# Kernel tuning notes

Hardware: AMD Instinct MI355X
Metric: run time of the kernel (lower is better)

## Reference

```python
import jax, jax.numpy as jnp
import numpy as np

EPS = 1e-5

def _conv3x3(x, w):
    # x: [n,c,h,w], w: [o,c,3,3], stride 1, padding 1 (SAME)
    return jax.lax.conv_general_dilated(x, w, (1, 1), 'SAME',
                                        dimension_numbers=('NCHW', 'OIHW', 'NCHW'))

def _bn(x, g, b, m, v):
    # inference-mode BatchNorm2d with running stats
    s = g / jnp.sqrt(v + EPS)
    return x * s[:, None, None] + (b - m * s)[:, None, None]

def _lrelu(x):
    return jnp.where(x > 0, x, 0.2 * x)

def _conv1x1(x, w, b):
    # w: [o,c] (1x1 conv kernel collapsed)
    return jnp.einsum('nchw,oc->nohw', x, w) + b[:, None, None]

def _conv_relu(x, w, g, b, m, v):
    return _lrelu(_bn(_conv3x3(x, w), g, b, m, v))

def _pam(f, Wq, bq, Wk, bk, Wv, bv, alpha):
    n, c, h, w = f.shape
    hw = h * w
    q = _conv1x1(f, Wq, bq).reshape(n, -1, hw)   # [n,cr,hw]
    k = _conv1x1(f, Wk, bk).reshape(n, -1, hw)   # [n,cr,hw]
    # attention[i,j] over spatial tokens, softmax along j
    attn = jax.nn.softmax(jnp.einsum('nci,ncj->nij', q, k), axis=-1)  # [n,hw,hw]
    v = _conv1x1(f, Wv, bv).reshape(n, c, hw)    # [n,c,hw]
    # torch: bmm(v, attn^T) -> out[:, :, i] = sum_j v[:, :, j] * attn[i, j]
    out = jnp.einsum('ncj,nij->nci', v, attn).reshape(n, c, h, w)
    return alpha * out + f

def _cam(f, W1, b1, W2, b2):
    s = jnp.mean(f, axis=(2, 3), keepdims=True)  # AdaptiveAvgPool2d(1)
    s = _lrelu(_conv1x1(s, W1, b1))
    s = jax.nn.sigmoid(_conv1x1(s, W2, b2))
    return f * s

def _upx2(x):
    n, c, h, w = x.shape
    return jax.image.resize(x, (n, c, 2 * h, 2 * w), 'bilinear')

def setup_inputs() -> dict:
    key = jax.random.key(0)
    ks = jax.random.split(key, 16)
    N, C, H, W_ = 4, 512, 64, 64
    CR, NC = C // 8, 64
    f32 = jnp.float32
    def nrm(k, shape, s=0.05):
        return jax.random.normal(k, shape, f32) * s
    return {
        'x': jax.random.normal(ks[0], (N, C, H, W_), f32),
        'W_pam_in': nrm(ks[1], (C, C, 3, 3)),
        'pam_gamma': jnp.ones((C,), f32), 'pam_beta': jnp.zeros((C,), f32),
        'pam_mean': nrm(ks[2], (C,)), 'pam_var': jax.random.uniform(ks[3], (C,), f32) + 0.5,
        'Wq': nrm(ks[4], (CR, C)), 'bq': jnp.zeros((CR,), f32),
        'Wk': nrm(ks[5], (CR, C)), 'bk': jnp.zeros((CR,), f32),
        'Wv': nrm(ks[6], (C, C)), 'bv': jnp.zeros((C,), f32),
        'alpha': nrm(ks[7], (1,), 1.0),
        'W_pam_out': nrm(ks[8], (NC, C)), 'b_pam_out': jnp.zeros((NC,), f32),
        'W_cam_in': nrm(ks[9], (C, C, 3, 3)),
        'cam_gamma': jnp.ones((C,), f32), 'cam_beta': jnp.zeros((C,), f32),
        'cam_mean': nrm(ks[10], (C,)), 'cam_var': jax.random.uniform(ks[11], (C,), f32) + 0.5,
        'Wc1': nrm(ks[12], (CR, C)), 'bc1': jnp.zeros((CR,), f32),
        'Wc2': nrm(ks[13], (C, CR)), 'bc2': jnp.zeros((C,), f32),
        'W_cam_out': nrm(ks[14], (NC, C)), 'b_cam_out': jnp.zeros((NC,), f32),
    }

def reference(x, W_pam_in, pam_gamma, pam_beta, pam_mean, pam_var,
              Wq, bq, Wk, bk, Wv, bv, alpha, W_pam_out, b_pam_out,
              W_cam_in, cam_gamma, cam_beta, cam_mean, cam_var,
              Wc1, bc1, Wc2, bc2, W_cam_out, b_cam_out):
    pam_feat = _conv_relu(x, W_pam_in, pam_gamma, pam_beta, pam_mean, pam_var)
    pam_feat = _pam(pam_feat, Wq, bq, Wk, bk, Wv, bv, alpha)
    pam_feat = _upx2(_conv1x1(pam_feat, W_pam_out, b_pam_out))
    cam_feat = _conv_relu(x, W_cam_in, cam_gamma, cam_beta, cam_mean, cam_var)
    cam_feat = _cam(cam_feat, Wc1, bc1, Wc2, bc2)
    cam_feat = _upx2(_conv1x1(cam_feat, W_cam_out, b_cam_out))
    return pam_feat + cam_feat
```

## Files before the change

kernel.cpp:

```cpp
#include <hip/hip_runtime.h>
#include <hip/hip_bf16.h>
#include <math.h>

#define N_  4
#define C_  512
#define H_  64
#define W_  64
#define HW_ 4096
#define CR_ 64
#define NC_ 64
#define EPSV 1e-5f

typedef __attribute__((ext_vector_type(8))) __bf16 bf16x8;
typedef __attribute__((ext_vector_type(4))) float f32x4;
typedef __hip_bfloat16 bf16s;

__device__ __forceinline__ unsigned short bfb(float f) {
    union { bf16s h; unsigned short u; } cv;
    cv.h = __float2bfloat16(f);
    return cv.u;
}

__device__ __forceinline__ float b2f(unsigned short h) {
    union { unsigned u; float f; } c; c.u = ((unsigned)h) << 16; return c.f;
}

__device__ __forceinline__ float ex2(float x) {
    return __builtin_amdgcn_exp2f(x);
}

__device__ __forceinline__ int swz8(int row, int ch) {
    return row * 64 + ((ch ^ (row & 7)) << 3);
}

__global__ __launch_bounds__(256) void k_prep(
    const float* __restrict__ x,
    const float* __restrict__ Wpam, const float* __restrict__ Wcam,
    const float* __restrict__ Wq, const float* __restrict__ Wk,
    const float* __restrict__ Wv, const float* __restrict__ Wpo,
    const float* __restrict__ Wco,
    bf16s* __restrict__ xbT,
    bf16s* __restrict__ wbp, bf16s* __restrict__ wbp2,
    bf16s* __restrict__ Wqb, bf16s* __restrict__ Wkb,
    bf16s* __restrict__ Wvb, bf16s* __restrict__ Wpob,
    bf16s* __restrict__ Wcob, float* __restrict__ s0)
{
    __shared__ float xs[64][65];
    const int b = blockIdx.x;
    if (b >= 19976) {
        const int idx = b - 19976;
        const int n   = idx >> 9;
        const int rem = idx & 511;
        const int p0  = (rem & 63) * 64;
        const int c0  = (rem >> 6) * 64;
        const int tid = threadIdx.x;
        for (int e = tid; e < 4096; e += 256) {
            int ci = e >> 6, pi = e & 63;
            xs[ci][pi] = x[((size_t)(n*C_ + c0 + ci))*HW_ + p0 + pi];
        }
        __syncthreads();
        for (int e = tid; e < 4096; e += 256) {
            int pi = e >> 6, ci = e & 63;
            xbT[((size_t)n*HW_ + p0 + pi)*C_ + c0 + ci] =
                __float2bfloat16(xs[ci][pi]);
        }
        return;
    }
    long e = (long)b * 256 + threadIdx.x;
    if (e < 2359296) {
        int c = e & 511; int r = e >> 9;
        int tap = r % 9; int o = r / 9;
        wbp[e] = __float2bfloat16(Wpam[((size_t)o*C_ + c)*9 + tap]);
        return;
    }
    e -= 2359296;
    if (e < 2359296) {
        int c = e & 511; int r = e >> 9;
        int tap = r % 9; int o = r / 9;
        wbp2[e] = __float2bfloat16(Wcam[((size_t)o*C_ + c)*9 + tap]);
        return;
    }
    e -= 2359296;
    if (e < 32768) { Wqb[e] = __float2bfloat16(Wq[e]); return; }
    e -= 32768;
    if (e < 32768) { Wkb[e] = __float2bfloat16(Wk[e]); return; }
    e -= 32768;
    if (e < 262144) { Wvb[e] = __float2bfloat16(Wv[e]); return; }
    e -= 262144;
    if (e < 32768) { Wpob[e] = __float2bfloat16(Wpo[e]); return; }
    e -= 32768;
    if (e < 32768) { Wcob[e] = __float2bfloat16(Wco[e]); return; }
    e -= 32768;
    if (e < 2048) s0[e] = 0.f;
}

__global__ __launch_bounds__(256, 3) void k_conv3x3_mfma(
    const bf16s* __restrict__ xbT,
    const bf16s* __restrict__ wb,  const bf16s* __restrict__ wb2,
    const float* __restrict__ gamma,  const float* __restrict__ beta,
    const float* __restrict__ mean,   const float* __restrict__ var,
    const float* __restrict__ gamma2, const float* __restrict__ beta2,
    const float* __restrict__ mean2,  const float* __restrict__ var2,
    bf16s* __restrict__ featT, bf16s* __restrict__ featT2,
    float* __restrict__ csum)
{
    __shared__ bf16s aL[3][128][36];
    __shared__ bf16s bL[132][36];
    const int tid = threadIdx.x;
    const int lid = blockIdx.x + (blockIdx.y << 5) + (blockIdx.z << 8);
    const int xcd = lid & 7;
    const int half = xcd >> 2;
    const int n    = xcd & 3;
    const int w8   = lid >> 3;
    const int o0 = (w8 >> 5) * 128;
    const int pt = w8 & 31;
    const int y0 = pt * 2;
    const bf16s* wbs = half ? wb2 : wb;
    const float* gm = half ? gamma2 : gamma;
    const float* bt = half ? beta2  : beta;
    const float* mn = half ? mean2  : mean;
    const float* vr = half ? var2   : var;
    bf16s* ft = half ? featT2 : featT;
    const int lane = tid & 63;
    const int wid  = tid >> 6;
    const int wr = wid >> 1, wc = wid & 1;
    const int lr = lane & 15, cb = lane >> 4;

    const int ao  = tid >> 2;
    const int ac  = (tid & 3) * 8;
    const int t0  = tid >> 2;
    const int t1  = t0 + 64;
    const int t2  = t0 + 128;
    const int ry1 = t1 >= 66 ? 1 : 0;
    const int xi1 = t1 - (ry1 ? 66 : 0);

    f32x4 acc[4][4];
#pragma unroll
    for (int i = 0; i < 4; ++i)
#pragma unroll
        for (int j = 0; j < 4; ++j) acc[i][j] = (f32x4){0.f,0.f,0.f,0.f};

    int4 pA0, pA1, pA2, pA3, pA4, pA5, pB0, pB1, pB2;

#define CONV_AADDR(DXI, OHALF, C0, DYI) \
    (const int4*)(wbs + ((size_t)(o0 + (OHALF) + ao)*9 + (DYI)*3 + (DXI))*C_ + (C0) + ac)

#define CONV_BLOAD(DST, RY, XI, C0, DYI, VALID)                               \
    {                                                                         \
        int row_ = y0 + (DYI) - 1 + (RY);                                     \
        int xc_  = (XI) - 1;                                                  \
        int4 v_ = {0,0,0,0};                                                  \
        if ((VALID) && row_ >= 0 && row_ < H_ && xc_ >= 0 && xc_ < W_)        \
            v_ = *(const int4*)(xbT +                                         \
                ((size_t)n*HW_ + row_*W_ + xc_)*C_ + (C0) + ac);              \
        DST = v_;                                                             \
    }

#define CONV_ISSUE(C0, DYI)                                                   \
    {                                                                         \
        pA0 = *CONV_AADDR(0,  0, C0, DYI);                                    \
        pA1 = *CONV_AADDR(0, 64, C0, DYI);                                    \
        pA2 = *CONV_AADDR(1,  0, C0, DYI);                                    \
        pA3 = *CONV_AADDR(1, 64, C0, DYI);                                    \
        pA4 = *CONV_AADDR(2,  0, C0, DYI);                                    \
        pA5 = *CONV_AADDR(2, 64, C0, DYI);                                    \
        CONV_BLOAD(pB0, 0, t0, C0, DYI, 1)                                    \
        CONV_BLOAD(pB1, ry1, xi1, C0, DYI, 1)                                 \
        CONV_BLOAD(pB2, 1, t2 - 66, C0, DYI, tid < 16)                        \
    }

    CONV_ISSUE(0, 0)
    int c0 = 0, dyi = 0;
    for (int it = 0; it < 48; ++it) {
        *(int4*)&aL[0][ao][ac]      = pA0;
        *(int4*)&aL[0][64 + ao][ac] = pA1;
        *(int4*)&aL[1][ao][ac]      = pA2;
        *(int4*)&aL[1][64 + ao][ac] = pA3;
        *(int4*)&aL[2][ao][ac]      = pA4;
        *(int4*)&aL[2][64 + ao][ac] = pA5;
        *(int4*)&bL[t0][ac] = pB0;
        *(int4*)&bL[t1][ac] = pB1;
        if (tid < 16) *(int4*)&bL[t2][ac] = pB2;
        __syncthreads();
        int nd = dyi + 1, nc = c0;
        if (nd == 3) { nd = 0; nc += 32; }
        if (it < 47) CONV_ISSUE(nc, nd)
#pragma unroll
        for (int dxi = 0; dxi < 3; ++dxi) {
            bf16x8 af[4], bfv[4];
#pragma unroll
            for (int fm = 0; fm < 4; ++fm)
                af[fm] = *(const bf16x8*)&aL[dxi][wr*64 + fm*16 + lr][cb*8];
#pragma unroll
            for (int fn = 0; fn < 4; ++fn) {
                int pg = wc*64 + fn*16 + lr;
                int ry = pg >> 6, xc = pg & 63;
                bfv[fn] = *(const bf16x8*)&bL[ry*66 + xc + dxi][cb*8];
            }
#pragma unroll
            for (int fm = 0; fm < 4; ++fm)
#pragma unroll
                for (int fn = 0; fn < 4; ++fn)
                    acc[fm][fn] = __builtin_amdgcn_mfma_f32_16x16x32_bf16(
                        af[fm], bfv[fn], acc[fm][fn], 0, 0, 0);
        }
        __syncthreads();
        c0 = nc; dyi = nd;
    }
#undef CONV_ISSUE
#undef CONV_BLOAD
#undef CONV_AADDR
#pragma unroll
    for (int fm = 0; fm < 4; ++fm) {
        float sc[4], sh[4];
        const int obase = o0 + wr*64 + fm*16 + cb*4;
#pragma unroll
        for (int r = 0; r < 4; ++r) {
            int o = obase + r;
            sc[r] = gm[o] * rsqrtf(vr[o] + EPSV);
            sh[r] = bt[o] - mn[o]*sc[r];
        }
        float ps[4] = {0.f, 0.f, 0.f, 0.f};
#pragma unroll
        for (int fn = 0; fn < 4; ++fn) {
            int pg = wc*64 + fn*16 + lr;
            int p  = pt*128 + pg;
            float vv[4];
#pragma unroll
            for (int r = 0; r < 4; ++r) {
                float t = fmaf(acc[fm][fn][r], sc[r], sh[r]);
                vv[r] = t > 0.f ? t : 0.2f*t;
                ps[r] += vv[r];
            }
            uint2 u;
            u.x = (unsigned)bfb(vv[0]) | ((unsigned)bfb(vv[1]) << 16);
            u.y = (unsigned)bfb(vv[2]) | ((unsigned)bfb(vv[3]) << 16);
            *(uint2*)&ft[((size_t)n*HW_ + p)*C_ + obase] = u;
        }
        if (half) {
#pragma unroll
            for (int r = 0; r < 4; ++r) {
                float s = ps[r];
                s += __shfl_xor(s, 1);
                s += __shfl_xor(s, 2);
                s += __shfl_xor(s, 4);
                s += __shfl_xor(s, 8);
                if (lr == 0) atomicAdd(&csum[n*C_ + obase + r], s);
            }
        }
    }
}

__global__ __launch_bounds__(256, 2) void k_gemm_qkv(
    const bf16s* __restrict__ Wqk, const bf16s* __restrict__ Wv,
    const bf16s* __restrict__ Bt,
    const float* __restrict__ bq, const float* __restrict__ bk,
    const float* __restrict__ bv,
    bf16s* __restrict__ qkb, bf16s* __restrict__ vb)
{
    __shared__ bf16s aL[64][36];
    __shared__ bf16s bL[256][36];
    const int tid = threadIdx.x;
    const int flat = blockIdx.x + (blockIdx.y << 4) + blockIdx.z * 160;
    const int k8 = flat & 7;
    const int n  = k8 >> 1;
    const int xh = k8 & 1;
    const int w8 = flat >> 3;
    const int yy = w8 % 10;
    const int p0 = ((((w8 / 10) << 1) | xh)) << 8;
    const bool isqk = (yy < 2);
    const int o0 = isqk ? yy*64 : (yy - 2)*64;
    const bf16s* A = isqk ? Wqk : Wv;
    const int lane = tid & 63;
    const int wid  = tid >> 6;
    const int lr = lane & 15, cb = lane >> 4;
    const int arow = tid >> 2, ach = (tid & 3) * 8;

    f32x4 acc[4][4];
#pragma unroll
    for (int i = 0; i < 4; ++i)
#pragma unroll
        for (int j = 0; j < 4; ++j) acc[i][j] = (f32x4){0.f,0.f,0.f,0.f};

    int4 pA, pB0, pB1, pB2, pB3;

#define GEMM_ISSUE(C0)                                                        \
    {                                                                         \
        pA = *(const int4*)&A[(size_t)(o0 + arow)*C_ + (C0) + ach];           \
        pB0 = *(const int4*)&Bt[((size_t)n*HW_ + p0 + arow      )*C_ + (C0) + ach]; \
        pB1 = *(const int4*)&Bt[((size_t)n*HW_ + p0 + arow +  64)*C_ + (C0) + ach]; \
        pB2 = *(const int4*)&Bt[((size_t)n*HW_ + p0 + arow + 128)*C_ + (C0) + ach]; \
        pB3 = *(const int4*)&Bt[((size_t)n*HW_ + p0 + arow + 192)*C_ + (C0) + ach]; \
    }

    GEMM_ISSUE(0)
    for (int c0 = 0; c0 < C_; c0 += 32) {
        *(int4*)&aL[arow][ach] = pA;
        *(int4*)&bL[arow      ][ach] = pB0;
        *(int4*)&bL[arow +  64][ach] = pB1;
        *(int4*)&bL[arow + 128][ach] = pB2;
        *(int4*)&bL[arow + 192][ach] = pB3;
        __syncthreads();
        if (c0 + 32 < C_) GEMM_ISSUE(c0 + 32)
        bf16x8 af[4], bfv[4];
#pragma unroll
        for (int fo = 0; fo < 4; ++fo)
            af[fo] = *(const bf16x8*)&aL[fo*16 + lr][cb*8];
#pragma unroll
        for (int fp = 0; fp < 4; ++fp)
            bfv[fp] = *(const bf16x8*)&bL[wid*64 + fp*16 + lr][cb*8];
#pragma unroll
        for (int fo = 0; fo < 4; ++fo)
#pragma unroll
            for (int fp = 0; fp < 4; ++fp)
                acc[fo][fp] = __builtin_amdgcn_mfma_f32_16x16x32_bf16(
                    af[fo], bfv[fp], acc[fo][fp], 0, 0, 0);
        __syncthreads();
    }
#undef GEMM_ISSUE
#pragma unroll
    for (int fo = 0; fo < 4; ++fo) {
        const int obase = o0 + fo*16 + cb*4;
        const bool isq = isqk && !(obase >> 6);
        const float* bp = isqk ? ((obase >> 6) ? bk : bq) : bv;
        const int bofs = isqk ? (obase & 63) : obase;
        float bv4[4];
#pragma unroll
        for (int r = 0; r < 4; ++r) bv4[r] = bp[bofs + r];
#pragma unroll
        for (int fp = 0; fp < 4; ++fp) {
            int p = p0 + wid*64 + fp*16 + lr;
            float v[4];
#pragma unroll
            for (int r = 0; r < 4; ++r) {
                v[r] = acc[fo][fp][r] + bv4[r];
                if (isq) v[r] *= 1.44269504f;
            }
            if (isqk) {
                uint2 u;
                u.x = (unsigned)bfb(v[0]) | ((unsigned)bfb(v[1]) << 16);
                u.y = (unsigned)bfb(v[2]) | ((unsigned)bfb(v[3]) << 16);
                size_t base = (((size_t)((obase >> 6) * N_ + n))*HW_ + p)*64
                              + (obase & 63);
                *(uint2*)&qkb[base] = u;
            } else {
#pragma unroll
                for (int r = 0; r < 4; ++r)
                    vb[((size_t)(n*C_ + obase + r))*HW_ + p] =
                        __float2bfloat16(v[r]);
            }
        }
    }
}

__global__ __launch_bounds__(256, 2) void k_gemm_tail(
    const bf16s* __restrict__ Wpob, const bf16s* __restrict__ Wcob,
    const bf16s* __restrict__ featT, const bf16s* __restrict__ featT2,
    const float* __restrict__ b_pam, const float* __restrict__ b_cam,
    const float* __restrict__ s0, const float* __restrict__ Wc1,
    const float* __restrict__ bc1, const float* __restrict__ Wc2,
    const float* __restrict__ bc2,
    float* __restrict__ pam_low, float* __restrict__ cam_low)
{
    __shared__ bf16s aL[64][36];
    __shared__ bf16s bL[256][36];
    __shared__ float s2s[C_];
    __shared__ float s1s[CR_];
    const int tid = threadIdx.x;
    const int half = blockIdx.y;
    const int n  = blockIdx.z;
    const int p0 = blockIdx.x * 256;
    const bf16s* A = half ? Wcob : Wpob;
    const bf16s* Bt = half ? featT2 : featT;
    const float* bias = half ? b_cam : b_pam;
    float* outp = half ? cam_low : pam_low;
    const int lane = tid & 63;
    const int wid  = tid >> 6;
    const int lr = lane & 15, cb = lane >> 4;
    const int arow = tid >> 2, ach = (tid & 3) * 8;

    if (half) {
        if (tid < CR_) {
            float a = 0.f;
            for (int c = 0; c < C_; ++c)
                a = fmaf(Wc1[(size_t)tid*C_ + c], s0[n*C_ + c] * (1.f/HW_), a);
            a += bc1[tid];
            s1s[tid] = a > 0.f ? a : 0.2f*a;
        }
        __syncthreads();
        for (int c = tid; c < C_; c += 256) {
            float bb = 0.f;
            for (int i = 0; i < CR_; ++i)
                bb = fmaf(Wc2[(size_t)c*CR_ + i], s1s[i], bb);
            bb += bc2[c];
            s2s[c] = 1.f / (1.f + __expf(-bb));
        }
        __syncthreads();
    }

    f32x4 acc[4][4];
#pragma unroll
    for (int i = 0; i < 4; ++i)
#pragma unroll
        for (int j = 0; j < 4; ++j) acc[i][j] = (f32x4){0.f,0.f,0.f,0.f};

    int4 pA, pB0, pB1, pB2, pB3;

#define GEMM_ISSUE(C0)                                                        \
    {                                                                         \
        pA = *(const int4*)&A[(size_t)arow*C_ + (C0) + ach];                  \
        pB0 = *(const int4*)&Bt[((size_t)n*HW_ + p0 + arow      )*C_ + (C0) + ach]; \
        pB1 = *(const int4*)&Bt[((size_t)n*HW_ + p0 + arow +  64)*C_ + (C0) + ach]; \
        pB2 = *(const int4*)&Bt[((size_t)n*HW_ + p0 + arow + 128)*C_ + (C0) + ach]; \
        pB3 = *(const int4*)&Bt[((size_t)n*HW_ + p0 + arow + 192)*C_ + (C0) + ach]; \
    }

    GEMM_ISSUE(0)
    for (int c0 = 0; c0 < C_; c0 += 32) {
        if (half) {
            const bf16s* sp = (const bf16s*)&pA;
            bf16s tmp[8];
#pragma unroll
            for (int u = 0; u < 8; ++u)
                tmp[u] = __float2bfloat16(
                    __bfloat162float(sp[u]) * s2s[c0 + ach + u]);
            *(int4*)&aL[arow][ach] = *(int4*)tmp;
        } else {
            *(int4*)&aL[arow][ach] = pA;
        }
        *(int4*)&bL[arow      ][ach] = pB0;
        *(int4*)&bL[arow +  64][ach] = pB1;
        *(int4*)&bL[arow + 128][ach] = pB2;
        *(int4*)&bL[arow + 192][ach] = pB3;
        __syncthreads();
        if (c0 + 32 < C_) GEMM_ISSUE(c0 + 32)
        bf16x8 af[4], bfv[4];
#pragma unroll
        for (int fo = 0; fo < 4; ++fo)
            af[fo] = *(const bf16x8*)&aL[fo*16 + lr][cb*8];
#pragma unroll
        for (int fp = 0; fp < 4; ++fp)
            bfv[fp] = *(const bf16x8*)&bL[wid*64 + fp*16 + lr][cb*8];
#pragma unroll
        for (int fo = 0; fo < 4; ++fo)
#pragma unroll
            for (int fp = 0; fp < 4; ++fp)
                acc[fo][fp] = __builtin_amdgcn_mfma_f32_16x16x32_bf16(
                    af[fo], bfv[fp], acc[fo][fp], 0, 0, 0);
        __syncthreads();
    }
#undef GEMM_ISSUE
#pragma unroll
    for (int fo = 0; fo < 4; ++fo) {
        const int obase = fo*16 + cb*4;
        float bv[4];
#pragma unroll
        for (int r = 0; r < 4; ++r) bv[r] = bias[obase + r];
#pragma unroll
        for (int fp = 0; fp < 4; ++fp) {
            int p = p0 + wid*64 + fp*16 + lr;
#pragma unroll
            for (int r = 0; r < 4; ++r)
                outp[((size_t)(n*NC_ + obase + r))*HW_ + p] =
                    acc[fo][fp][r] + bv[r];
        }
    }
}

__global__ __launch_bounds__(256, 4) void k_pv_mfma(
    const bf16s* __restrict__ qb, const bf16s* __restrict__ kb,
    const bf16s* __restrict__ vb, const float* __restrict__ alpha,
    bf16s* __restrict__ featT)
{
    __shared__ bf16s ks[2][4096];
    __shared__ bf16s ps[2][4096];
    __shared__ float sfl[2][64];
    __shared__ float lfin[64];
    const int tid = threadIdx.x;
    const int lid = blockIdx.x + (blockIdx.y << 6) + (blockIdx.z << 8);
    const int k8  = lid & 7;
    const int n   = k8 >> 1;
    const int cc0 = (((lid >> 3) & 1) * 2 + (k8 & 1)) << 7;
    const int i0  = (lid >> 4) << 6;
    const int lane = tid & 63;
    const int wid  = tid >> 6;
    const int lr = lane & 15, cb = lane >> 4;

    for (int e = tid; e < 512; e += 256) {
        int row = e >> 3, ch = e & 7;
        *(int4*)&ks[0][swz8(row, ch)] =
            *(const int4*)&qb[((size_t)n*HW_ + i0 + row)*CR_ + ch*8];
    }
    const int krow = tid >> 3, kch = tid & 7;
    const bf16s* kbase = kb + (size_t)n*HW_*CR_ + kch*8;
    int4 kreg0 = *(const int4*)(kbase + (size_t)krow*CR_);
    int4 kreg1 = *(const int4*)(kbase + (size_t)(krow + 32)*CR_);
    __syncthreads();
    bf16x8 bq[2];
#pragma unroll
    for (int kk = 0; kk < 2; ++kk)
        bq[kk] = *(const bf16x8*)&ks[0][swz8(wid*16 + lr, kk*4 + cb)];

    const float al = alpha[0];
    __syncthreads();
    *(int4*)&ks[0][swz8(krow, kch)] = kreg0;
    *(int4*)&ks[0][swz8(krow + 32, kch)] = kreg1;
    kreg0 = *(const int4*)(kbase + (size_t)(64 + krow)*CR_);
    kreg1 = *(const int4*)(kbase + (size_t)(64 + krow + 32)*CR_);
    __syncthreads();

    f32x4 acc[2][4];
#pragma unroll
    for (int i = 0; i < 2; ++i)
#pragma unroll
        for (int j = 0; j < 4; ++j) acc[i][j] = (f32x4){0.f,0.f,0.f,0.f};

    float m_run = -INFINITY, l_run = 0.f;

    const bf16s* vbase = vb + ((size_t)(n*C_ + cc0 + wid*32))*HW_;
    bf16x8 vc0, vc1, vc2, vc3, vn0, vn1, vn2, vn3;

    for (int jt = 0; jt < 64; ++jt) {
        const bf16s* vj = vbase + jt*64;
        vn0 = *(const bf16x8*)(vj + (size_t)(     lr)*HW_      + cb*8);
        vn1 = *(const bf16x8*)(vj + (size_t)(16 + lr)*HW_      + cb*8);
        vn2 = *(const bf16x8*)(vj + (size_t)(     lr)*HW_ + 32 + cb*8);
        vn3 = *(const bf16x8*)(vj + (size_t)(16 + lr)*HW_ + 32 + cb*8);
        if (jt > 0) {
            const float* fs = sfl[(jt - 1) & 1];
            const bf16s* pp = ps[(jt - 1) & 1];
            bf16x8 pa[4];
#pragma unroll
            for (int fi = 0; fi < 4; ++fi) {
                const float f = fs[fi*16 + lr];
#pragma unroll
                for (int r = 0; r < 4; ++r) {
                    acc[0][fi][r] *= f;
                    acc[1][fi][r] *= f;
                }
            }
#pragma unroll
            for (int fi = 0; fi < 4; ++fi)
                pa[fi] = *(const bf16x8*)&pp[swz8(fi*16 + lr, cb)];
            __builtin_amdgcn_s_setprio(1);
#pragma unroll
            for (int fi = 0; fi < 4; ++fi) {
                acc[0][fi] = __builtin_amdgcn_mfma_f32_16x16x32_bf16(
                    vc0, pa[fi], acc[0][fi], 0, 0, 0);
                acc[1][fi] = __builtin_amdgcn_mfma_f32_16x16x32_bf16(
                    vc1, pa[fi], acc[1][fi], 0, 0, 0);
            }
            __builtin_amdgcn_s_setprio(0);
#pragma unroll
            for (int fi = 0; fi < 4; ++fi)
                pa[fi] = *(const bf16x8*)&pp[swz8(fi*16 + lr, 4 + cb)];
            __builtin_amdgcn_s_setprio(1);
#pragma unroll
            for (int fi = 0; fi < 4; ++fi) {
                acc[0][fi] = __builtin_amdgcn_mfma_f32_16x16x32_bf16(
                    vc2, pa[fi], acc[0][fi], 0, 0, 0);
                acc[1][fi] = __builtin_amdgcn_mfma_f32_16x16x32_bf16(
                    vc3, pa[fi], acc[1][fi], 0, 0, 0);
            }
            __builtin_amdgcn_s_setprio(0);
        }
        {
            const bf16s* kst = ks[jt & 1];
            bf16s* pst = ps[jt & 1];
            f32x4 sv0 = (f32x4){0.f,0.f,0.f,0.f};
            f32x4 sv1 = (f32x4){0.f,0.f,0.f,0.f};
            f32x4 sv2 = (f32x4){0.f,0.f,0.f,0.f};
            f32x4 sv3 = (f32x4){0.f,0.f,0.f,0.f};
            sv0 = __builtin_amdgcn_mfma_f32_16x16x32_bf16(
                *(const bf16x8*)&kst[swz8(     lr, cb)], bq[0], sv0, 0, 0, 0);
            sv0 = __builtin_amdgcn_mfma_f32_16x16x32_bf16(
                *(const bf16x8*)&kst[swz8(     lr, 4 + cb)], bq[1], sv0, 0, 0, 0);
            sv1 = __builtin_amdgcn_mfma_f32_16x16x32_bf16(
                *(const bf16x8*)&kst[swz8(16 + lr, cb)], bq[0], sv1, 0, 0, 0);
            sv1 = __builtin_amdgcn_mfma_f32_16x16x32_bf16(
                *(const bf16x8*)&kst[swz8(16 + lr, 4 + cb)], bq[1], sv1, 0, 0, 0);
            sv2 = __builtin_amdgcn_mfma_f32_16x16x32_bf16(
                *(const bf16x8*)&kst[swz8(32 + lr, cb)], bq[0], sv2, 0, 0, 0);
            sv2 = __builtin_amdgcn_mfma_f32_16x16x32_bf16(
                *(const bf16x8*)&kst[swz8(32 + lr, 4 + cb)], bq[1], sv2, 0, 0, 0);
            sv3 = __builtin_amdgcn_mfma_f32_16x16x32_bf16(
                *(const bf16x8*)&kst[swz8(48 + lr, cb)], bq[0], sv3, 0, 0, 0);
            sv3 = __builtin_amdgcn_mfma_f32_16x16x32_bf16(
                *(const bf16x8*)&kst[swz8(48 + lr, 4 + cb)], bq[1], sv3, 0, 0, 0);
            float tmax = sv0[0];
#pragma unroll
            for (int r = 0; r < 4; ++r) {
                tmax = fmaxf(tmax, sv0[r]); tmax = fmaxf(tmax, sv1[r]);
                tmax = fmaxf(tmax, sv2[r]); tmax = fmaxf(tmax, sv3[r]);
            }
            tmax = fmaxf(tmax, __shfl_xor(tmax, 16));
            tmax = fmaxf(tmax, __shfl_xor(tmax, 32));
            float fsc;
            if (tmax > m_run + 11.5f) {
                fsc = ex2(m_run - tmax);
                m_run = tmax;
            } else {
                fsc = 1.f;
            }
            float tsum = 0.f;
#define PV_PACK(SV, FJ)                                                       \
            {                                                                 \
                float p0_ = ex2(SV[0] - m_run), p1_ = ex2(SV[1] - m_run);     \
                float p2_ = ex2(SV[2] - m_run), p3_ = ex2(SV[3] - m_run);     \
                tsum += (p0_ + p1_) + (p2_ + p3_);                            \
                uint2 u;                                                      \
                u.x = (unsigned)bfb(p0_) | ((unsigned)bfb(p1_) << 16);        \
                u.y = (unsigned)bfb(p2_) | ((unsigned)bfb(p3_) << 16);        \
                *(uint2*)&pst[swz8(wid*16 + lr, FJ*2 + (cb >> 1)) + (cb & 1)*4] = u; \
            }
            PV_PACK(sv0, 0)
            PV_PACK(sv1, 1)
            PV_PACK(sv2, 2)
            PV_PACK(sv3, 3)
#undef PV_PACK
            tsum += __shfl_xor(tsum, 16);
            tsum += __shfl_xor(tsum, 32);
            l_run = l_run * fsc + tsum;
            if (cb == 0) sfl[jt & 1][wid*16 + lr] = fsc;
        }
        if (jt < 63) {
            *(int4*)&ks[(jt + 1) & 1][swz8(krow, kch)] = kreg0;
            *(int4*)&ks[(jt + 1) & 1][swz8(krow + 32, kch)] = kreg1;
            if (jt < 62) {
                kreg0 = *(const int4*)(kbase + (size_t)((jt+2)*64 + krow)*CR_);
                kreg1 = *(const int4*)(kbase + (size_t)((jt+2)*64 + krow + 32)*CR_);
            }
        }
        vc0 = vn0; vc1 = vn1; vc2 = vn2; vc3 = vn3;
        __syncthreads();
    }
    if (cb == 0) lfin[wid*16 + lr] = l_run;
    {
        const float* fs = sfl[1];
        const bf16s* pp = ps[1];
        bf16x8 pa[4];
#pragma unroll
        for (int fi = 0; fi < 4; ++fi) {
            const float f = fs[fi*16 + lr];
#pragma unroll
            for (int r = 0; r < 4; ++r) {
                acc[0][fi][r] *= f;
                acc[1][fi][r] *= f;
            }
        }
#pragma unroll
        for (int fi = 0; fi < 4; ++fi)
            pa[fi] = *(const bf16x8*)&pp[swz8(fi*16 + lr, cb)];
#pragma unroll
        for (int fi = 0; fi < 4; ++fi) {
            acc[0][fi] = __builtin_amdgcn_mfma_f32_16x16x32_bf16(
                vc0, pa[fi], acc[0][fi], 0, 0, 0);
            acc[1][fi] = __builtin_amdgcn_mfma_f32_16x16x32_bf16(
                vc1, pa[fi], acc[1][fi], 0, 0, 0);
        }
#pragma unroll
        for (int fi = 0; fi < 4; ++fi)
            pa[fi] = *(const bf16x8*)&pp[swz8(fi*16 + lr, 4 + cb)];
#pragma unroll
        for (int fi = 0; fi < 4; ++fi) {
            acc[0][fi] = __builtin_amdgcn_mfma_f32_16x16x32_bf16(
                vc2, pa[fi], acc[0][fi], 0, 0, 0);
            acc[1][fi] = __builtin_amdgcn_mfma_f32_16x16x32_bf16(
                vc3, pa[fi], acc[1][fi], 0, 0, 0);
        }
    }
    __syncthreads();
#pragma unroll
    for (int fc2 = 0; fc2 < 2; ++fc2) {
        const int ccl = wid*32 + fc2*16 + cb*4;
#pragma unroll
        for (int fi = 0; fi < 4; ++fi) {
            const int p = i0 + fi*16 + lr;
            const float rv = al / lfin[fi*16 + lr];
            bf16s* fb = &featT[((size_t)n*HW_ + p)*C_ + cc0 + ccl];
            uint2 fv = *(const uint2*)fb;
            float f0 = b2f((unsigned short)(fv.x & 0xffff));
            float f1 = b2f((unsigned short)(fv.x >> 16));
            float f2 = b2f((unsigned short)(fv.y & 0xffff));
            float f3 = b2f((unsigned short)(fv.y >> 16));
            float v0 = fmaf(rv, acc[fc2][fi][0], f0);
            float v1 = fmaf(rv, acc[fc2][fi][1], f1);
            float v2 = fmaf(rv, acc[fc2][fi][2], f2);
            float v3 = fmaf(rv, acc[fc2][fi][3], f3);
            uint2 u;
            u.x = (unsigned)bfb(v0) | ((unsigned)bfb(v1) << 16);
            u.y = (unsigned)bfb(v2) | ((unsigned)bfb(v3) << 16);
            *(uint2*)fb = u;
        }
    }
}

__global__ __launch_bounds__(256) void k_up(
    const float* __restrict__ pl, const float* __restrict__ cl,
    float* __restrict__ out)
{
    int idx = blockIdx.x * 256 + threadIdx.x;
    int ox = idx & 127; int rest = idx >> 7;
    int oy = rest & 127; rest >>= 7;
    int o  = rest & 63;  int n = rest >> 6;
    float fy = oy*0.5f - 0.25f;
    float fx = ox*0.5f - 0.25f;
    int y0 = (int)floorf(fy); float wy = fy - y0;
    int x0 = (int)floorf(fx); float wx = fx - x0;
    int y0c = y0 < 0 ? 0 : y0;      int y1c = y0+1 > 63 ? 63 : y0+1;
    int x0c = x0 < 0 ? 0 : x0;      int x1c = x0+1 > 63 ? 63 : x0+1;
    const float* a = pl + ((size_t)(n*NC_ + o))*HW_;
    const float* b = cl + ((size_t)(n*NC_ + o))*HW_;
    float v00 = a[y0c*64+x0c] + b[y0c*64+x0c];
    float v01 = a[y0c*64+x1c] + b[y0c*64+x1c];
    float v10 = a[y1c*64+x0c] + b[y1c*64+x0c];
    float v11 = a[y1c*64+x1c] + b[y1c*64+x1c];
    out[idx] = (1.f-wy)*((1.f-wx)*v00 + wx*v01) + wy*((1.f-wx)*v10 + wx*v11);
}

extern "C" void kernel_launch(void* const* d_in, const int* in_sizes, int n_in,
                              void* d_out, int out_size, void* d_ws, size_t ws_size,
                              hipStream_t stream)
{
    const float* x         = (const float*)d_in[0];
    const float* W_pam_in  = (const float*)d_in[1];
    const float* pam_g     = (const float*)d_in[2];
    const float* pam_b     = (const float*)d_in[3];
    const float* pam_m     = (const float*)d_in[4];
    const float* pam_v     = (const float*)d_in[5];
    const float* Wq        = (const float*)d_in[6];
    const float* bq        = (const float*)d_in[7];
    const float* Wk        = (const float*)d_in[8];
    const float* bk        = (const float*)d_in[9];
    const float* Wv        = (const float*)d_in[10];
    const float* bv        = (const float*)d_in[11];
    const float* alpha     = (const float*)d_in[12];
    const float* W_pam_out = (const float*)d_in[13];
    const float* b_pam_out = (const float*)d_in[14];
    const float* W_cam_in  = (const float*)d_in[15];
    const float* cam_g     = (const float*)d_in[16];
    const float* cam_b     = (const float*)d_in[17];
    const float* cam_m     = (const float*)d_in[18];
    const float* cam_v     = (const float*)d_in[19];
    const float* Wc1       = (const float*)d_in[20];
    const float* bc1       = (const float*)d_in[21];
    const float* Wc2       = (const float*)d_in[22];
    const float* bc2       = (const float*)d_in[23];
    const float* W_cam_out = (const float*)d_in[24];
    const float* b_cam_out = (const float*)d_in[25];

    float* pam_low = (float*)d_ws;
    float* s0      = pam_low + 1048576;
    bf16s* xbT     = (bf16s*)(s0 + 2048);
    bf16s* featTb  = xbT + 8388608;
    bf16s* featTb2 = featTb + 8388608;
    bf16s* vb      = featTb2 + 8388608;
    bf16s* qb      = vb + 8388608;
    bf16s* kb      = qb + 1048576;
    bf16s* wbp     = kb + 1048576;
    bf16s* wbp2    = wbp + 2359296;
    bf16s* Wqb     = wbp2 + 2359296;
    bf16s* Wkb     = Wqb + 32768;
    bf16s* Wvb     = Wkb + 32768;
    bf16s* Wpob    = Wvb + 262144;
    bf16s* Wcob    = Wpob + 32768;
    float* cam_low = (float*)qb;

    dim3 b256(256);
    k_prep<<<dim3(22024), b256, 0, stream>>>(
        x, W_pam_in, W_cam_in, Wq, Wk, Wv, W_pam_out, W_cam_out,
        xbT, wbp, wbp2, Wqb, Wkb, Wvb, Wpob, Wcob, s0);
    k_conv3x3_mfma<<<dim3(32,8,4), b256, 0, stream>>>(
        xbT, wbp, wbp2, pam_g, pam_b, pam_m, pam_v,
        cam_g, cam_b, cam_m, cam_v, featTb, featTb2, s0);
    k_gemm_qkv<<<dim3(16,10,4), b256, 0, stream>>>(
        Wqb, Wvb, featTb, bq, bk, bv, qb, vb);
    k_pv_mfma<<<dim3(64,4,4), b256, 0, stream>>>(
        qb, kb, vb, alpha, featTb);
    k_gemm_tail<<<dim3(16,2,4), b256, 0, stream>>>(
        Wpob, Wcob, featTb, featTb2, b_pam_out, b_cam_out,
        s0, Wc1, bc1, Wc2, bc2, pam_low, cam_low);
    k_up<<<dim3(16384), b256, 0, stream>>>(pam_low, cam_low, (float*)d_out);
}
```

Baseline: 406.5 us.

## Stage 4-row input halo once per channel chunk, read weights directly from global

The 3x3 conv main loop now stages a 4-row by 66-column input halo tile in shared memory once per 32-channel chunk and reuses it across all three dy taps. Before, a 2-row tile was reloaded for each dy. Weight fragments are no longer staged in LDS; each wave loads them straight from global memory for every dy/dx tap. This cuts LDS traffic, barriers and loop iterations, but puts uncached, unprefetched global weight loads on the MFMA critical path.

```diff
diff --git a/kernel.cpp b/kernel.cpp
--- a/kernel.cpp
+++ b/kernel.cpp
@@ -104,8 +104,7 @@
     bf16s* __restrict__ featT, bf16s* __restrict__ featT2,
     float* __restrict__ csum)
 {
-    __shared__ bf16s aL[3][128][36];
-    __shared__ bf16s bL[132][36];
+    __shared__ bf16s bL[264][36];
     const int tid = threadIdx.x;
     const int lid = blockIdx.x + (blockIdx.y << 5) + (blockIdx.z << 8);
     const int xcd = lid & 7;
@@ -126,90 +125,80 @@
     const int wr = wid >> 1, wc = wid & 1;
     const int lr = lane & 15, cb = lane >> 4;
 
-    const int ao  = tid >> 2;
-    const int ac  = (tid & 3) * 8;
-    const int t0  = tid >> 2;
-    const int t1  = t0 + 64;
-    const int t2  = t0 + 128;
-    const int ry1 = t1 >= 66 ? 1 : 0;
-    const int xi1 = t1 - (ry1 ? 66 : 0);
-
     f32x4 acc[4][4];
 #pragma unroll
     for (int i = 0; i < 4; ++i)
 #pragma unroll
         for (int j = 0; j < 4; ++j) acc[i][j] = (f32x4){0.f,0.f,0.f,0.f};
 
-    int4 pA0, pA1, pA2, pA3, pA4, pA5, pB0, pB1, pB2;
-
-#define CONV_AADDR(DXI, OHALF, C0, DYI) \
-    (const int4*)(wbs + ((size_t)(o0 + (OHALF) + ao)*9 + (DYI)*3 + (DXI))*C_ + (C0) + ac)
-
-#define CONV_BLOAD(DST, RY, XI, C0, DYI, VALID)                               \
+    int4 pB0, pB1, pB2, pB3, pB4;
+
+#define CONV_BLOADK(DST, K, C0)                                               \
     {                                                                         \
-        int row_ = y0 + (DYI) - 1 + (RY);                                     \
-        int xc_  = (XI) - 1;                                                  \
+        int e_ = tid + (K)*256;                                               \
         int4 v_ = {0,0,0,0};                                                  \
-        if ((VALID) && row_ >= 0 && row_ < H_ && xc_ >= 0 && xc_ < W_)        \
-            v_ = *(const int4*)(xbT +                                         \
-                ((size_t)n*HW_ + row_*W_ + xc_)*C_ + (C0) + ac);              \
+        if ((K) < 4 || e_ < 1056) {                                           \
+            int cb2_ = e_ & 3; int t_ = e_ >> 2;                              \
+            int ry_ = t_ / 66, xi_ = t_ % 66;                                 \
+            int row_ = y0 - 1 + ry_;                                          \
+            int xc_  = xi_ - 1;                                               \
+            if (row_ >= 0 && row_ < H_ && xc_ >= 0 && xc_ < W_)               \
+                v_ = *(const int4*)(xbT +                                     \
+                    ((size_t)n*HW_ + row_*W_ + xc_)*C_ + (C0) + cb2_*8);      \
+        }                                                                     \
         DST = v_;                                                             \
     }
 
-#define CONV_ISSUE(C0, DYI)                                                   \
+#define CONV_BISSUE(C0)                                                       \
+    CONV_BLOADK(pB0, 0, C0) CONV_BLOADK(pB1, 1, C0)                           \
+    CONV_BLOADK(pB2, 2, C0) CONV_BLOADK(pB3, 3, C0)                           \
+    CONV_BLOADK(pB4, 4, C0)
+
+#define CONV_BCOMMITK(SRC, K)                                                 \
     {                                                                         \
-        pA0 = *CONV_AADDR(0,  0, C0, DYI);                                    \
-        pA1 = *CONV_AADDR(0, 64, C0, DYI);                                    \
-        pA2 = *CONV_AADDR(1,  0, C0, DYI);                                    \
-        pA3 = *CONV_AADDR(1, 64, C0, DYI);                                    \
-        pA4 = *CONV_AADDR(2,  0, C0, DYI);                                    \
-        pA5 = *CONV_AADDR(2, 64, C0, DYI);                                    \
-        CONV_BLOAD(pB0, 0, t0, C0, DYI, 1)                                    \
-        CONV_BLOAD(pB1, ry1, xi1, C0, DYI, 1)                                 \
-        CONV_BLOAD(pB2, 1, t2 - 66, C0, DYI, tid < 16)                        \
-    }
-
-    CONV_ISSUE(0, 0)
-    int c0 = 0, dyi = 0;
-    for (int it = 0; it < 48; ++it) {
-        *(int4*)&aL[0][ao][ac]      = pA0;
-        *(int4*)&aL[0][64 + ao][ac] = pA1;
-        *(int4*)&aL[1][ao][ac]      = pA2;
-        *(int4*)&aL[1][64 + ao][ac] = pA3;
-        *(int4*)&aL[2][ao][ac]      = pA4;
-        *(int4*)&aL[2][64 + ao][ac] = pA5;
-        *(int4*)&bL[t0][ac] = pB0;
-        *(int4*)&bL[t1][ac] = pB1;
-        if (tid < 16) *(int4*)&bL[t2][ac] = pB2;
-        __syncthreads();
-        int nd = dyi + 1, nc = c0;
-        if (nd == 3) { nd = 0; nc += 32; }
-        if (it < 47) CONV_ISSUE(nc, nd)
-#pragma unroll
-        for (int dxi = 0; dxi < 3; ++dxi) {
-            bf16x8 af[4], bfv[4];
-#pragma unroll
-            for (int fm = 0; fm < 4; ++fm)
-                af[fm] = *(const bf16x8*)&aL[dxi][wr*64 + fm*16 + lr][cb*8];
-#pragma unroll
-            for (int fn = 0; fn < 4; ++fn) {
-                int pg = wc*64 + fn*16 + lr;
-                int ry = pg >> 6, xc = pg & 63;
-                bfv[fn] = *(const bf16x8*)&bL[ry*66 + xc + dxi][cb*8];
-            }
-#pragma unroll
-            for (int fm = 0; fm < 4; ++fm)
-#pragma unroll
-                for (int fn = 0; fn < 4; ++fn)
-                    acc[fm][fn] = __builtin_amdgcn_mfma_f32_16x16x32_bf16(
-                        af[fm], bfv[fn], acc[fm][fn], 0, 0, 0);
-        }
-        __syncthreads();
-        c0 = nc; dyi = nd;
-    }
-#undef CONV_ISSUE
-#undef CONV_BLOAD
-#undef CONV_AADDR
+        int e_ = tid + (K)*256;                                               \
+        if ((K) < 4 || e_ < 1056) {                                           \
+            int cb2_ = e_ & 3; int t_ = e_ >> 2;                              \
+            *(int4*)&bL[t_][cb2_*8] = SRC;                                    \
+        }                                                                     \
+    }
+
+    CONV_BISSUE(0)
+    for (int c0 = 0; c0 < C_; c0 += 32) {
+        CONV_BCOMMITK(pB0, 0) CONV_BCOMMITK(pB1, 1)
+        CONV_BCOMMITK(pB2, 2) CONV_BCOMMITK(pB3, 3)
+        CONV_BCOMMITK(pB4, 4)
+        __syncthreads();
+        if (c0 + 32 < C_) CONV_BISSUE(c0 + 32)
+#pragma unroll
+        for (int dyi = 0; dyi < 3; ++dyi) {
+#pragma unroll
+            for (int dxi = 0; dxi < 3; ++dxi) {
+                bf16x8 af[4], bfv[4];
+#pragma unroll
+                for (int fm = 0; fm < 4; ++fm)
+                    af[fm] = *(const bf16x8*)(wbs +
+                        ((size_t)(o0 + wr*64 + fm*16 + lr)*9 + dyi*3 + dxi)*C_
+                        + c0 + cb*8);
+#pragma unroll
+                for (int fn = 0; fn < 4; ++fn) {
+                    int pg = wc*64 + fn*16 + lr;
+                    int ry = pg >> 6, xc = pg & 63;
+                    bfv[fn] = *(const bf16x8*)&bL[(ry + dyi)*66 + xc + dxi][cb*8];
+                }
+#pragma unroll
+                for (int fm = 0; fm < 4; ++fm)
+#pragma unroll
+                    for (int fn = 0; fn < 4; ++fn)
+                        acc[fm][fn] = __builtin_amdgcn_mfma_f32_16x16x32_bf16(
+                            af[fm], bfv[fn], acc[fm][fn], 0, 0, 0);
+            }
+        }
+        __syncthreads();
+    }
+#undef CONV_BISSUE
+#undef CONV_BLOADK
+#undef CONV_BCOMMITK
 #pragma unroll
     for (int fm = 0; fm < 4; ++fm) {
         float sc[4], sh[4];
```

Measured after the change: 656.9 us. 61.6% more time.
